# Kernel optimization log

Measured on AMD Instinct MI355X. Metric: run time of the kernel, lower is better.

## Reference

```python
import jax, jax.numpy as jnp
import numpy as np

B, T, D, HD = 4, 4096, 1024, 64

def setup_inputs() -> dict:
    key = jax.random.key(0)
    kx, kq, kk, kv = jax.random.split(key, 4)
    s = 1.0 / np.sqrt(D)
    return {
        "x": jax.random.normal(kx, (B, T, D), dtype=jnp.float32),
        "wq": jax.random.uniform(kq, (HD, D), jnp.float32, -s, s),
        "wk": jax.random.uniform(kk, (HD, D), jnp.float32, -s, s),
        "wv": jax.random.uniform(kv, (HD, D), jnp.float32, -s, s),
    }

def reference(x, wq, wk, wv):
    # Linear(D, headDim, bias=False): y = x @ W.T with W of shape [headDim, D]
    Q = jnp.einsum('btD,dD->btd', x, wq)
    K = jnp.einsum('bsD,dD->bsd', x, wk)
    V = jnp.einsum('bsD,dD->bsd', x, wv)
    head_dim = wq.shape[0]
    logits = jnp.einsum('btd,bsd->bts', Q, K) / jnp.sqrt(jnp.float32(head_dim))
    attn = jax.nn.softmax(logits, axis=-1)
    return jnp.einsum('bts,bsd->btd', attn, V)
```

## Files before the change

kernel.cpp:

```cpp
#include <hip/hip_runtime.h>
#include <math.h>

#define TLEN 4096
#define BD   1024
#define HDIM 64
#define NB   4

typedef __attribute__((ext_vector_type(8))) short bf16x8;
typedef __attribute__((ext_vector_type(4))) float f32x4;

typedef const __attribute__((address_space(1))) unsigned char* gp_t;
typedef __attribute__((address_space(3))) unsigned char* lp_t;

__device__ __forceinline__ void async_cp16(const void* g, void* l) {
    __builtin_amdgcn_global_load_lds((gp_t)g, (lp_t)l, 16, 0, 0);
}

__device__ __forceinline__ unsigned short f2bf(float f) {
    union { float f; unsigned u; } v; v.f = f;
    unsigned r = v.u + 0x7FFF + ((v.u >> 16) & 1);
    return (unsigned short)(r >> 16);
}

__device__ __forceinline__ bf16x8 cvt8(const float4 a, const float4 b) {
    bf16x8 r;
    r[0] = (short)f2bf(a.x); r[1] = (short)f2bf(a.y);
    r[2] = (short)f2bf(a.z); r[3] = (short)f2bf(a.w);
    r[4] = (short)f2bf(b.x); r[5] = (short)f2bf(b.y);
    r[6] = (short)f2bf(b.z); r[7] = (short)f2bf(b.w);
    return r;
}

__global__ __launch_bounds__(256) void wconv_kernel(
    const float* __restrict__ wq, const float* __restrict__ wk,
    const float* __restrict__ wv, unsigned short* __restrict__ wbf)
{
    const int r = blockIdx.x;
    const float* src = (r < 64) ? wq : (r < 128) ? wk : wv;
    const int rr = r & 63;
    const int c  = threadIdx.x * 4;
    float4 a = *(const float4*)&src[(size_t)rr * BD + c];
    uint2 o;
    o.x = (unsigned)f2bf(a.x) | ((unsigned)f2bf(a.y) << 16);
    o.y = (unsigned)f2bf(a.z) | ((unsigned)f2bf(a.w) << 16);
    *(uint2*)&wbf[(size_t)r * BD + c] = o;
}

__global__ __launch_bounds__(256, 1) void qkv_kernel(
    const float* __restrict__ x,
    const unsigned short* __restrict__ wbf,
    unsigned short* __restrict__ Qb,
    unsigned short* __restrict__ Kb,
    unsigned short* __restrict__ Vt)
{
    const int r0   = blockIdx.x * 32;
    const int tid  = threadIdx.x;
    const int lane = tid & 63;
    const int w    = tid >> 6;
    const int g    = lane >> 4;
    const int c    = lane & 15;

    __shared__ __align__(16) unsigned short xb[2][32 * 64];
    __shared__ __align__(16) unsigned short wsh[2][192 * 64];
    __shared__ __align__(16) unsigned short vtr[64][40];

    f32x4 acc[3][2];
    #pragma unroll
    for (int t = 0; t < 3; ++t)
        #pragma unroll
        for (int rg = 0; rg < 2; ++rg) acc[t][rg] = (f32x4){0.f, 0.f, 0.f, 0.f};

    float4 xr0, xr1;

    #define STAGE_W(buf, k0s)                                                   \
        {                                                                       \
            _Pragma("unroll")                                                   \
            for (int ii = 0; ii < 6; ++ii) {                                    \
                const int L   = ii * 256 + tid;                                 \
                const int row = L >> 3;                                         \
                const int jl  = (L & 7) ^ (row & 7);                            \
                async_cp16(&wbf[(size_t)row * BD + (k0s) + jl * 8],             \
                           &wsh[buf][L * 8]);                                   \
            }                                                                   \
        }
    #define LOAD_X(k0s)                                                         \
        {                                                                       \
            const int row = tid >> 3;                                           \
            const int jl  = (tid & 7) ^ (row & 7);                              \
            const float* s = &x[(size_t)(r0 + row) * BD + (k0s) + jl * 8];      \
            xr0 = *(const float4*)s;                                            \
            xr1 = *(const float4*)(s + 4);                                      \
        }
    #define WRITE_X(buf)                                                        \
        { *(bf16x8*)&xb[buf][tid * 8] = cvt8(xr0, xr1); }

    STAGE_W(0, 0)
    LOAD_X(0)
    WRITE_X(0)

    for (int it = 0; it < 16; ++it) {
        const int cb = it & 1;
        __syncthreads();

        if (it < 15) {
            STAGE_W(cb ^ 1, (it + 1) * 64)
            LOAD_X((it + 1) * 64)
        }

        #pragma unroll
        for (int h = 0; h < 2; ++h) {
            const int slot = ((h * 4 + g) ^ (c & 7)) * 8;
            bf16x8 aX[2], bW[3];
            #pragma unroll
            for (int rg = 0; rg < 2; ++rg)
                aX[rg] = *(const bf16x8*)&xb[cb][(rg * 16 + c) * 64 + slot];
            #pragma unroll
            for (int t = 0; t < 3; ++t)
                bW[t] = *(const bf16x8*)&wsh[cb][((w * 3 + t) * 16 + c) * 64 + slot];
            #pragma unroll
            for (int t = 0; t < 3; ++t)
                #pragma unroll
                for (int rg = 0; rg < 2; ++rg)
                    acc[t][rg] = __builtin_amdgcn_mfma_f32_16x16x32_bf16(
                        aX[rg], bW[t], acc[t][rg], 0, 0, 0);
        }

        if (it < 15) WRITE_X(cb ^ 1)
    }

    const float qscale = 0.18033688f;
    const int   bb     = r0 / TLEN;
    const int   trow   = r0 % TLEN;
    #pragma unroll
    for (int t = 0; t < 3; ++t) {
        const int m = w * 3 + t;
        #pragma unroll
        for (int rg = 0; rg < 2; ++rg)
            #pragma unroll
            for (int i = 0; i < 4; ++i) {
                const int row = rg * 16 + g * 4 + i;
                if (m < 4)
                    Qb[(size_t)(r0 + row) * HDIM + m * 16 + c]
                        = f2bf(acc[t][rg][i] * qscale);
                else if (m < 8)
                    Kb[(size_t)(r0 + row) * HDIM + (m - 4) * 16 + c]
                        = f2bf(acc[t][rg][i]);
                else
                    vtr[(m - 8) * 16 + c][row] = f2bf(acc[t][rg][i]);
            }
    }
    __syncthreads();
    {
        const int d    = tid >> 2;
        const int part = tid & 3;
        uint4 v0 = *(const uint4*)&vtr[d][part * 8];
        unsigned short* dst = Vt + (size_t)bb * HDIM * TLEN + (size_t)d * TLEN
                            + trow + part * 8;
        *(uint4*)&dst[0] = v0;
    }
    #undef STAGE_W
    #undef LOAD_X
    #undef WRITE_X
}

template <int KEYS>
__global__ __launch_bounds__(128, 1) void attn_kernel(
    const unsigned short* __restrict__ Qb,
    const unsigned short* __restrict__ Kb,
    const unsigned short* __restrict__ Vt,
    float* __restrict__ O1, float* __restrict__ Ml, float* __restrict__ out)
{
    const int b     = blockIdx.y;
    const int q0    = blockIdx.x * 64;
    const int split = blockIdx.z;
    const int sbase = split * KEYS;

    const unsigned short* Qp = Qb + (size_t)b * TLEN * HDIM;
    const unsigned short* Kp = Kb + (size_t)b * TLEN * HDIM + (size_t)sbase * HDIM;
    const unsigned short* Vp = Vt + (size_t)b * HDIM * TLEN + sbase;

    const int tid  = threadIdx.x;
    const int lane = tid & 63;
    const int w    = tid >> 6;
    const int g    = lane >> 4;
    const int c    = lane & 15;

    __shared__ __align__(16) unsigned short ks[2][4096];
    __shared__ __align__(16) unsigned short vs[2][4096];
    __shared__ __align__(16) unsigned short pp[64][72];

    bf16x8 qA[2][2];
    #pragma unroll
    for (int h = 0; h < 2; ++h)
        #pragma unroll
        for (int kk = 0; kk < 2; ++kk)
            qA[h][kk] = *(const bf16x8*)
                &Qp[(size_t)(q0 + w * 32 + h * 16 + c) * HDIM + kk * 32 + g * 8];

    float lsum[2][4] = {};
    f32x4 oacc[2][4];
    #pragma unroll
    for (int h = 0; h < 2; ++h)
        #pragma unroll
        for (int t = 0; t < 4; ++t) oacc[h][t] = (f32x4){0.f, 0.f, 0.f, 0.f};

    const int nt = KEYS / 64;

    #pragma unroll
    for (int ii = 0; ii < 4; ++ii) {
        const int L   = ii * 128 + tid;
        const int row = L >> 3;
        const int jl  = (L & 7) ^ (row & 7);
        async_cp16(&Kp[(size_t)row * HDIM + jl * 8], &ks[0][L * 8]);
        async_cp16(&Vp[(size_t)row * TLEN + jl * 8], &vs[0][L * 8]);
    }

    for (int it = 0; it < nt; ++it) {
        const int cb = it & 1;
        __syncthreads();

        if (it + 1 < nt) {
            const int s0  = (it + 1) * 64;
            const int nb2 = cb ^ 1;
            #pragma unroll
            for (int ii = 0; ii < 4; ++ii) {
                const int L   = ii * 128 + tid;
                const int row = L >> 3;
                const int jl  = (L & 7) ^ (row & 7);
                async_cp16(&Kp[(size_t)(s0 + row) * HDIM + jl * 8], &ks[nb2][L * 8]);
                async_cp16(&Vp[(size_t)row * TLEN + s0 + jl * 8],   &vs[nb2][L * 8]);
            }
        }

        f32x4 sacc[2][4];
        #pragma unroll
        for (int h = 0; h < 2; ++h)
            #pragma unroll
            for (int t = 0; t < 4; ++t) sacc[h][t] = (f32x4){0.f, 0.f, 0.f, 0.f};
        #pragma unroll
        for (int t = 0; t < 4; ++t) {
            const int r  = 16 * t + c;
            const int j0 = g ^ (r & 7);
            bf16x8 kB0 = *(const bf16x8*)&ks[cb][(r * 8 + j0) * 8];
            bf16x8 kB1 = *(const bf16x8*)&ks[cb][(r * 8 + (j0 ^ 4)) * 8];
            #pragma unroll
            for (int h = 0; h < 2; ++h) {
                sacc[h][t] = __builtin_amdgcn_mfma_f32_16x16x32_bf16(
                    qA[h][0], kB0, sacc[h][t], 0, 0, 0);
                sacc[h][t] = __builtin_amdgcn_mfma_f32_16x16x32_bf16(
                    qA[h][1], kB1, sacc[h][t], 0, 0, 0);
            }
        }

        #pragma unroll
        for (int h = 0; h < 2; ++h)
            #pragma unroll
            for (int i = 0; i < 4; ++i) {
                float p0 = __builtin_amdgcn_exp2f(sacc[h][0][i]);
                float p1 = __builtin_amdgcn_exp2f(sacc[h][1][i]);
                float p2 = __builtin_amdgcn_exp2f(sacc[h][2][i]);
                float p3 = __builtin_amdgcn_exp2f(sacc[h][3][i]);
                unsigned u0 = __float_as_uint(p0) & 0xffff0000u;
                unsigned u1 = __float_as_uint(p1) & 0xffff0000u;
                unsigned u2 = __float_as_uint(p2) & 0xffff0000u;
                unsigned u3 = __float_as_uint(p3) & 0xffff0000u;
                lsum[h][i] += (__uint_as_float(u0) + __uint_as_float(u1))
                            + (__uint_as_float(u2) + __uint_as_float(u3));
                unsigned short* pr = &pp[w * 32 + h * 16 + g * 4 + i][c];
                pr[0]  = (unsigned short)(u0 >> 16);
                pr[16] = (unsigned short)(u1 >> 16);
                pr[32] = (unsigned short)(u2 >> 16);
                pr[48] = (unsigned short)(u3 >> 16);
            }

        bf16x8 pA[2][2];
        #pragma unroll
        for (int h = 0; h < 2; ++h) {
            pA[h][0] = *(const bf16x8*)&pp[w * 32 + h * 16 + c][g * 8];
            pA[h][1] = *(const bf16x8*)&pp[w * 32 + h * 16 + c][32 + g * 8];
        }
        #pragma unroll
        for (int t = 0; t < 4; ++t) {
            const int r  = 16 * t + c;
            const int j0 = g ^ (r & 7);
            bf16x8 vB0 = *(const bf16x8*)&vs[cb][(r * 8 + j0) * 8];
            bf16x8 vB1 = *(const bf16x8*)&vs[cb][(r * 8 + (j0 ^ 4)) * 8];
            #pragma unroll
            for (int h = 0; h < 2; ++h) {
                oacc[h][t] = __builtin_amdgcn_mfma_f32_16x16x32_bf16(
                    pA[h][0], vB0, oacc[h][t], 0, 0, 0);
                oacc[h][t] = __builtin_amdgcn_mfma_f32_16x16x32_bf16(
                    pA[h][1], vB1, oacc[h][t], 0, 0, 0);
            }
        }
    }

    #pragma unroll
    for (int h = 0; h < 2; ++h)
        #pragma unroll
        for (int i = 0; i < 4; ++i) {
            lsum[h][i] += __shfl_xor(lsum[h][i], 1);
            lsum[h][i] += __shfl_xor(lsum[h][i], 2);
            lsum[h][i] += __shfl_xor(lsum[h][i], 4);
            lsum[h][i] += __shfl_xor(lsum[h][i], 8);
        }

    #pragma unroll
    for (int h = 0; h < 2; ++h) {
        const size_t orow = (size_t)(b * TLEN + q0 + w * 32 + h * 16 + g * 4);
        if (KEYS == TLEN) {
            #pragma unroll
            for (int i = 0; i < 4; ++i) {
                const float inv = 1.0f / lsum[h][i];
                #pragma unroll
                for (int t = 0; t < 4; ++t)
                    out[(orow + i) * HDIM + 16 * t + c] = oacc[h][t][i] * inv;
            }
        } else {
            float* Od = (split == 0)
                ? out : O1 + (size_t)(split - 1) * NB * TLEN * HDIM;
            #pragma unroll
            for (int i = 0; i < 4; ++i)
                #pragma unroll
                for (int t = 0; t < 4; ++t)
                    Od[(orow + i) * HDIM + 16 * t + c] = oacc[h][t][i];
            if (c == 0) {
                #pragma unroll
                for (int i = 0; i < 4; ++i)
                    Ml[(size_t)(split * NB + b) * TLEN
                       + q0 + w * 32 + h * 16 + g * 4 + i] = lsum[h][i];
            }
        }
    }
}

__global__ __launch_bounds__(256) void merge_kernel(
    float* __restrict__ out, const float* __restrict__ O1,
    const float* __restrict__ Ml)
{
    const int idx  = blockIdx.x * 256 + threadIdx.x;
    const int row  = idx >> 4;
    const int col4 = (idx & 15) * 4;
    const int b    = row >> 12;
    const int t    = row & (TLEN - 1);
    float l = 0.f;
    #pragma unroll
    for (int s = 0; s < 4; ++s) l += Ml[(size_t)(s * NB + b) * TLEN + t];
    const float inv = 1.0f / l;
    float4 a = *(const float4*)&out[(size_t)row * HDIM + col4];
    #pragma unroll
    for (int s = 1; s < 4; ++s) {
        float4 p = *(const float4*)
            &O1[(size_t)(s - 1) * NB * TLEN * HDIM + (size_t)row * HDIM + col4];
        a.x += p.x; a.y += p.y; a.z += p.z; a.w += p.w;
    }
    a.x *= inv; a.y *= inv; a.z *= inv; a.w *= inv;
    *(float4*)&out[(size_t)row * HDIM + col4] = a;
}

extern "C" void kernel_launch(void* const* d_in, const int* in_sizes, int n_in,
                              void* d_out, int out_size, void* d_ws, size_t ws_size,
                              hipStream_t stream)
{
    (void)in_sizes; (void)n_in; (void)out_size;
    const float* x  = (const float*)d_in[0];
    const float* wq = (const float*)d_in[1];
    const float* wk = (const float*)d_in[2];
    const float* wv = (const float*)d_in[3];
    float* out = (float*)d_out;

    unsigned short* wbf = (unsigned short*)d_out;
    unsigned short* Qbf = (unsigned short*)d_ws;
    unsigned short* Kbf = Qbf + (size_t)NB * TLEN * HDIM;
    unsigned short* Vtb = Kbf + (size_t)NB * TLEN * HDIM;
    float* Ml = (float*)((char*)d_ws + (size_t)3 * NB * TLEN * HDIM * 2);
    float* O1 = Ml + (size_t)4 * NB * TLEN;
    const size_t ws_need = (size_t)3 * NB * TLEN * HDIM * 2
                         + (size_t)4 * NB * TLEN * 4
                         + (size_t)3 * NB * TLEN * HDIM * 4;
    const bool use_split = ws_size >= ws_need;

    wconv_kernel<<<dim3(192), 256, 0, stream>>>(wq, wk, wv, wbf);
    qkv_kernel<<<dim3(NB * TLEN / 32), 256, 0, stream>>>(x, wbf, Qbf, Kbf, Vtb);

    if (use_split) {
        attn_kernel<TLEN / 4><<<dim3(TLEN / 64, NB, 4), 128, 0, stream>>>(
            Qbf, Kbf, Vtb, O1, Ml, out);
        merge_kernel<<<dim3(NB * TLEN * 16 / 256), 256, 0, stream>>>(out, O1, Ml);
    } else {
        attn_kernel<TLEN><<<dim3(TLEN / 64, NB, 1), 128, 0, stream>>>(
            Qbf, Kbf, Vtb, O1, Ml, out);
    }
}
```

Measured before the change: 171.6 us.

## Widen attention block to 128 queries and transpose QK MFMA for packed P stores

Doubles the attention workgroup to 256 threads covering 128 queries, so each K/V tile staged in LDS is reused by twice as many queries and the per-thread async copy count is halved. Swaps the MFMA operands in the QK^T product so each lane holds four consecutive keys for one query. That lets P be written to shared memory as packed 8-byte stores instead of scalar 2-byte stores, and shrinks the row-sum reduction to two shuffles. The cost is half as many workgroups, which may hurt occupancy and load balance across CUs, plus a larger pp buffer in LDS.

```diff
diff --git a/kernel.cpp b/kernel.cpp
--- a/kernel.cpp
+++ b/kernel.cpp
@@ -164,14 +164,14 @@
 }
 
 template <int KEYS>
-__global__ __launch_bounds__(128, 1) void attn_kernel(
+__global__ __launch_bounds__(256, 2) void attn_kernel(
     const unsigned short* __restrict__ Qb,
     const unsigned short* __restrict__ Kb,
     const unsigned short* __restrict__ Vt,
     float* __restrict__ O1, float* __restrict__ Ml, float* __restrict__ out)
 {
     const int b     = blockIdx.y;
-    const int q0    = blockIdx.x * 64;
+    const int q0    = blockIdx.x * 128;
     const int split = blockIdx.z;
     const int sbase = split * KEYS;
 
@@ -187,17 +187,17 @@
 
     __shared__ __align__(16) unsigned short ks[2][4096];
     __shared__ __align__(16) unsigned short vs[2][4096];
-    __shared__ __align__(16) unsigned short pp[64][72];
-
-    bf16x8 qA[2][2];
+    __shared__ __align__(16) unsigned short pp[128][72];
+
+    bf16x8 qB[2][2];
     #pragma unroll
     for (int h = 0; h < 2; ++h)
         #pragma unroll
         for (int kk = 0; kk < 2; ++kk)
-            qA[h][kk] = *(const bf16x8*)
+            qB[h][kk] = *(const bf16x8*)
                 &Qp[(size_t)(q0 + w * 32 + h * 16 + c) * HDIM + kk * 32 + g * 8];
 
-    float lsum[2][4] = {};
+    float lsum[2] = {0.f, 0.f};
     f32x4 oacc[2][4];
     #pragma unroll
     for (int h = 0; h < 2; ++h)
@@ -207,8 +207,8 @@
     const int nt = KEYS / 64;
 
     #pragma unroll
-    for (int ii = 0; ii < 4; ++ii) {
-        const int L   = ii * 128 + tid;
+    for (int ii = 0; ii < 2; ++ii) {
+        const int L   = ii * 256 + tid;
         const int row = L >> 3;
         const int jl  = (L & 7) ^ (row & 7);
         async_cp16(&Kp[(size_t)row * HDIM + jl * 8], &ks[0][L * 8]);
@@ -223,8 +223,8 @@
             const int s0  = (it + 1) * 64;
             const int nb2 = cb ^ 1;
             #pragma unroll
-            for (int ii = 0; ii < 4; ++ii) {
-                const int L   = ii * 128 + tid;
+            for (int ii = 0; ii < 2; ++ii) {
+                const int L   = ii * 256 + tid;
                 const int row = L >> 3;
                 const int jl  = (L & 7) ^ (row & 7);
                 async_cp16(&Kp[(size_t)(s0 + row) * HDIM + jl * 8], &ks[nb2][L * 8]);
@@ -241,37 +241,38 @@
         for (int t = 0; t < 4; ++t) {
             const int r  = 16 * t + c;
             const int j0 = g ^ (r & 7);
-            bf16x8 kB0 = *(const bf16x8*)&ks[cb][(r * 8 + j0) * 8];
-            bf16x8 kB1 = *(const bf16x8*)&ks[cb][(r * 8 + (j0 ^ 4)) * 8];
+            bf16x8 kA0 = *(const bf16x8*)&ks[cb][(r * 8 + j0) * 8];
+            bf16x8 kA1 = *(const bf16x8*)&ks[cb][(r * 8 + (j0 ^ 4)) * 8];
             #pragma unroll
             for (int h = 0; h < 2; ++h) {
                 sacc[h][t] = __builtin_amdgcn_mfma_f32_16x16x32_bf16(
-                    qA[h][0], kB0, sacc[h][t], 0, 0, 0);
+                    kA0, qB[h][0], sacc[h][t], 0, 0, 0);
                 sacc[h][t] = __builtin_amdgcn_mfma_f32_16x16x32_bf16(
-                    qA[h][1], kB1, sacc[h][t], 0, 0, 0);
-            }
-        }
-
-        #pragma unroll
-        for (int h = 0; h < 2; ++h)
-            #pragma unroll
-            for (int i = 0; i < 4; ++i) {
-                float p0 = __builtin_amdgcn_exp2f(sacc[h][0][i]);
-                float p1 = __builtin_amdgcn_exp2f(sacc[h][1][i]);
-                float p2 = __builtin_amdgcn_exp2f(sacc[h][2][i]);
-                float p3 = __builtin_amdgcn_exp2f(sacc[h][3][i]);
+                    kA1, qB[h][1], sacc[h][t], 0, 0, 0);
+            }
+        }
+
+        #pragma unroll
+        for (int h = 0; h < 2; ++h) {
+            const int qloc = w * 32 + h * 16 + c;
+            #pragma unroll
+            for (int t = 0; t < 4; ++t) {
+                float p0 = __builtin_amdgcn_exp2f(sacc[h][t][0]);
+                float p1 = __builtin_amdgcn_exp2f(sacc[h][t][1]);
+                float p2 = __builtin_amdgcn_exp2f(sacc[h][t][2]);
+                float p3 = __builtin_amdgcn_exp2f(sacc[h][t][3]);
                 unsigned u0 = __float_as_uint(p0) & 0xffff0000u;
                 unsigned u1 = __float_as_uint(p1) & 0xffff0000u;
                 unsigned u2 = __float_as_uint(p2) & 0xffff0000u;
                 unsigned u3 = __float_as_uint(p3) & 0xffff0000u;
-                lsum[h][i] += (__uint_as_float(u0) + __uint_as_float(u1))
-                            + (__uint_as_float(u2) + __uint_as_float(u3));
-                unsigned short* pr = &pp[w * 32 + h * 16 + g * 4 + i][c];
-                pr[0]  = (unsigned short)(u0 >> 16);
-                pr[16] = (unsigned short)(u1 >> 16);
-                pr[32] = (unsigned short)(u2 >> 16);
-                pr[48] = (unsigned short)(u3 >> 16);
-            }
+                lsum[h] += (__uint_as_float(u0) + __uint_as_float(u1))
+                         + (__uint_as_float(u2) + __uint_as_float(u3));
+                uint2 pk;
+                pk.x = (u0 >> 16) | u1;
+                pk.y = (u2 >> 16) | u3;
+                *(uint2*)&pp[qloc][16 * t + g * 4] = pk;
+            }
+        }
 
         bf16x8 pA[2][2];
         #pragma unroll
@@ -296,14 +297,10 @@
     }
 
     #pragma unroll
-    for (int h = 0; h < 2; ++h)
-        #pragma unroll
-        for (int i = 0; i < 4; ++i) {
-            lsum[h][i] += __shfl_xor(lsum[h][i], 1);
-            lsum[h][i] += __shfl_xor(lsum[h][i], 2);
-            lsum[h][i] += __shfl_xor(lsum[h][i], 4);
-            lsum[h][i] += __shfl_xor(lsum[h][i], 8);
-        }
+    for (int h = 0; h < 2; ++h) {
+        lsum[h] += __shfl_xor(lsum[h], 16);
+        lsum[h] += __shfl_xor(lsum[h], 32);
+    }
 
     #pragma unroll
     for (int h = 0; h < 2; ++h) {
@@ -311,7 +308,7 @@
         if (KEYS == TLEN) {
             #pragma unroll
             for (int i = 0; i < 4; ++i) {
-                const float inv = 1.0f / lsum[h][i];
+                const float inv = 1.0f / __shfl(lsum[h], g * 4 + i);
                 #pragma unroll
                 for (int t = 0; t < 4; ++t)
                     out[(orow + i) * HDIM + 16 * t + c] = oacc[h][t][i] * inv;
@@ -324,12 +321,9 @@
                 #pragma unroll
                 for (int t = 0; t < 4; ++t)
                     Od[(orow + i) * HDIM + 16 * t + c] = oacc[h][t][i];
-            if (c == 0) {
-                #pragma unroll
-                for (int i = 0; i < 4; ++i)
-                    Ml[(size_t)(split * NB + b) * TLEN
-                       + q0 + w * 32 + h * 16 + g * 4 + i] = lsum[h][i];
-            }
+            if (lane < 16)
+                Ml[(size_t)(split * NB + b) * TLEN
+                   + q0 + w * 32 + h * 16 + lane] = lsum[h];
         }
     }
 }
@@ -384,11 +378,11 @@
     qkv_kernel<<<dim3(NB * TLEN / 32), 256, 0, stream>>>(x, wbf, Qbf, Kbf, Vtb);
 
     if (use_split) {
-        attn_kernel<TLEN / 4><<<dim3(TLEN / 64, NB, 4), 128, 0, stream>>>(
+        attn_kernel<TLEN / 4><<<dim3(TLEN / 128, NB, 4), 256, 0, stream>>>(
             Qbf, Kbf, Vtb, O1, Ml, out);
         merge_kernel<<<dim3(NB * TLEN * 16 / 256), 256, 0, stream>>>(out, O1, Ml);
     } else {
-        attn_kernel<TLEN><<<dim3(TLEN / 64, NB, 1), 128, 0, stream>>>(
+        attn_kernel<TLEN><<<dim3(TLEN / 128, NB, 1), 256, 0, stream>>>(
             Qbf, Kbf, Vtb, O1, Ml, out);
     }
 }
```

New measurement: 153.7 us. 10.4% less time.
